# Kernel optimization log

Hardware: AMD Instinct MI355X
Metric: run time of the kernel (lower is better)

The kernel has to match this reference:

```python
import jax, jax.numpy as jnp
import numpy as np

N, L, D, H, HIST = 4, 1024, 1024, 16, 128
HD = D // H          # head_dim = 64
SCALE = D ** 0.5     # note: original scales by sqrt(model_dim), not sqrt(head_dim)


def _band_mask():
    # get_mask: tril XOR tril(diag=-history_len) -> True inside the causal band.
    # masked_fill fills where mask is True, so pass the complement (True outside band).
    r = jnp.arange(L)[:, None]
    c = jnp.arange(L)[None, :]
    band = (c <= r) & (c > r - HIST)  # band of width HIST incl. diagonal
    return jnp.broadcast_to(~band, (N, 1, L, L))


def setup_inputs() -> dict:
    key = jax.random.key(0)
    ks = jax.random.split(key, 8)
    s = 0.02
    return {
        "values": jax.random.normal(ks[0], (N, L, D), jnp.float32),
        "keys": jax.random.normal(ks[1], (N, L, D), jnp.float32),
        "query": jax.random.normal(ks[2], (N, L, D), jnp.float32),
        "mask": _band_mask(),
        "Wv": jax.random.normal(ks[3], (HD, HD), jnp.float32) * s,
        "Wk": jax.random.normal(ks[4], (HD, HD), jnp.float32) * s,
        "Wq": jax.random.normal(ks[5], (HD, HD), jnp.float32) * s,
        "Wo": jax.random.normal(ks[6], (D, D), jnp.float32) * s,
        "bo": jax.random.normal(ks[7], (D,), jnp.float32) * s,
    }


def reference(values, keys, query, mask, Wv, Wk, Wq, Wo, bo):
    n, qlen, _ = query.shape
    # split heads and apply per-head linear projections (nn.Linear: x @ W.T)
    v = values.reshape(n, -1, H, HD) @ Wv.T
    k = keys.reshape(n, -1, H, HD) @ Wk.T
    q = query.reshape(n, qlen, H, HD) @ Wq.T
    # full energy [n, h, q, k]
    energy = jnp.einsum('nqhd,nkhd->nhqk', q, k)
    energy = jnp.where(mask, jnp.float32(-1e20), energy)
    scores = jax.nn.softmax(energy / SCALE, axis=-1)
    # NOTE: faithful to original einsum 'nhql,nlhd->nlhd' (reduces over q):
    # attention[n,l,h,d] = (sum_q scores[n,h,q,l]) * v[n,l,h,d]
    attention = jnp.einsum('nhql,nlhd->nlhd', scores, v)
    out = attention.reshape(n, qlen, D) @ Wo.T + bo
    return out
```

## Files before the change

### kernel.cpp

```cpp
#include <hip/hip_runtime.h>
#include <hip/hip_bf16.h>
#include <math.h>


using short8 = __attribute__((ext_vector_type(8))) short;
using f32x4  = __attribute__((ext_vector_type(4))) float;

__device__ __forceinline__ unsigned short f2bf(float x) {
    unsigned u = __float_as_uint(x);
    u += 0x7FFFu + ((u >> 16) & 1u);
    return (unsigned short)(u >> 16);
}

__global__ __launch_bounds__(256) void k_prep0(const float* __restrict__ Wq,
                                               const float* __restrict__ Wk,
                                               const float* __restrict__ Wv,
                                               const float4* __restrict__ Wo4,
                                               float* __restrict__ w,
                                               ushort4* __restrict__ wob4,
                                               unsigned short* __restrict__ Mrb,
                                               unsigned short* __restrict__ Wvb) {
    const int b = blockIdx.x, tid = threadIdx.x;
    if (b < 1024) {
        int idx = b * 256 + tid;
        float4 v = Wo4[idx];
        ushort4 o; o.x = f2bf(v.x); o.y = f2bf(v.y);
        o.z = f2bf(v.z); o.w = f2bf(v.w);
        wob4[idx] = o;
        if (b < 256) w[b * 256 + tid] = 0.f;
    } else {
        int idx = (b - 1024) * 256 + tid;
        int e = idx >> 6, f = idx & 63;
        float s = 0.f;
#pragma unroll 8
        for (int d = 0; d < 64; ++d) s = fmaf(Wq[d * 64 + e], Wk[d * 64 + f], s);
        Mrb[idx] = f2bf(s * (1.0f / 32.0f));
        Wvb[idx] = f2bf(Wv[idx]);
    }
}

__global__ __launch_bounds__(256) void k_kp(const float* __restrict__ keys,
                                            const unsigned short* __restrict__ Mrb,
                                            unsigned short* __restrict__ kk2p) {
    const int tid = threadIdx.x;
    const long R0 = (long)blockIdx.x * 64;
    const int wv = tid >> 6, lane = tid & 63;
    const int m = lane & 15, ksel = (lane >> 4) * 8;

    const float* ka = keys + (R0 + wv * 16 + m) * 64;
    short8 af[2];
#pragma unroll
    for (int ch = 0; ch < 2; ++ch) {
        float4 x0 = *reinterpret_cast<const float4*>(ka + ch * 32 + ksel);
        float4 x1 = *reinterpret_cast<const float4*>(ka + ch * 32 + ksel + 4);
        short8 a;
        a[0] = (short)f2bf(x0.x); a[1] = (short)f2bf(x0.y);
        a[2] = (short)f2bf(x0.z); a[3] = (short)f2bf(x0.w);
        a[4] = (short)f2bf(x1.x); a[5] = (short)f2bf(x1.y);
        a[6] = (short)f2bf(x1.z); a[7] = (short)f2bf(x1.w);
        af[ch] = a;
    }

    f32x4 acc[4];
#pragma unroll
    for (int fc = 0; fc < 4; ++fc) {
        acc[fc] = f32x4{0.f, 0.f, 0.f, 0.f};
#pragma unroll
        for (int ch = 0; ch < 2; ++ch) {
            short8 bf = *reinterpret_cast<const short8*>(
                Mrb + (size_t)(fc * 16 + m) * 64 + ch * 32 + ksel);
            acc[fc] = __builtin_amdgcn_mfma_f32_16x16x32_bf16(af[ch], bf, acc[fc], 0, 0, 0);
        }
    }

    const long rowb = R0 + wv * 16 + (lane >> 4) * 4;
#pragma unroll
    for (int reg = 0; reg < 4; ++reg) {
        long rg = rowb + reg;
        int hh = (int)(rg & 15);
        int ll = (int)((rg >> 4) & 1023);
        int nn = (int)(rg >> 14);
        unsigned short* orow = kk2p + ((size_t)((nn * 16 + hh) * 1024 + ll)) * 64;
#pragma unroll
        for (int fc = 0; fc < 4; ++fc)
            orow[fc * 16 + m] = f2bf(acc[fc][reg]);
    }
}

__global__ __launch_bounds__(256) void k_w2(const float* __restrict__ query,
                                            const unsigned short* __restrict__ kk2p,
                                            float* __restrict__ w) {
    __shared__ float wloc[192];

    const int tid  = threadIdx.x;
    const int b    = blockIdx.x;
    const int nh   = b & 63;
    const int tile = b >> 6;
    const int h    = nh & 15;
    const int n    = nh >> 4;
    const int t0   = tile * 64;

    if (tid < 192) wloc[tid] = 0.f;
    __syncthreads();

    const int wv = tid >> 6, lane = tid & 63;
    const int m = lane & 15, q4 = lane >> 4, ksel = q4 * 8;

    const float* qrow = query + ((size_t)(n * 1024 + t0 + wv * 16 + m)) * 1024 + h * 64;
    short8 af0, af1;
    {
        float4 x0 = *reinterpret_cast<const float4*>(qrow + ksel);
        float4 x1 = *reinterpret_cast<const float4*>(qrow + ksel + 4);
        float4 y0 = *reinterpret_cast<const float4*>(qrow + 32 + ksel);
        float4 y1 = *reinterpret_cast<const float4*>(qrow + 32 + ksel + 4);
        af0[0] = (short)f2bf(x0.x); af0[1] = (short)f2bf(x0.y);
        af0[2] = (short)f2bf(x0.z); af0[3] = (short)f2bf(x0.w);
        af0[4] = (short)f2bf(x1.x); af0[5] = (short)f2bf(x1.y);
        af0[6] = (short)f2bf(x1.z); af0[7] = (short)f2bf(x1.w);
        af1[0] = (short)f2bf(y0.x); af1[1] = (short)f2bf(y0.y);
        af1[2] = (short)f2bf(y0.z); af1[3] = (short)f2bf(y0.w);
        af1[4] = (short)f2bf(y1.x); af1[5] = (short)f2bf(y1.y);
        af1[6] = (short)f2bf(y1.z); af1[7] = (short)f2bf(y1.w);
    }

    const unsigned short* kb = kk2p + (size_t)nh * 1024 * 64;

    f32x4 acc[12];
#pragma unroll
    for (int ni = 0; ni < 12; ++ni) {
        int l = t0 - 127 + ni * 16 + m;
        int lc = min(max(l, 0), 1023);
        const unsigned short* kp = kb + (size_t)lc * 64 + ksel;
        short8 b0 = *reinterpret_cast<const short8*>(kp);
        short8 b1 = *reinterpret_cast<const short8*>(kp + 32);
        f32x4 a = f32x4{0.f, 0.f, 0.f, 0.f};
        a = __builtin_amdgcn_mfma_f32_16x16x32_bf16(af0, b0, a, 0, 0, 0);
        a = __builtin_amdgcn_mfma_f32_16x16x32_bf16(af1, b1, a, 0, 0, 0);
        acc[ni] = a;
    }

    const int rbase = wv * 16 + q4 * 4;
    float rs[4] = {0.f, 0.f, 0.f, 0.f};
#pragma unroll
    for (int ni = 0; ni < 12; ++ni) {
        const int c = ni * 16 + m;
#pragma unroll
        for (int reg = 0; reg < 4; ++reg) {
            const int rlw = rbase + reg;
            bool valid = (c >= rlw) && (c <= rlw + 127) && (c + t0 >= 127);
            float e = valid ? __expf(acc[ni][reg]) : 0.f;
            acc[ni][reg] = e;
            rs[reg] += e;
        }
    }
#pragma unroll
    for (int reg = 0; reg < 4; ++reg) {
#pragma unroll
        for (int mm = 1; mm < 16; mm <<= 1) rs[reg] += __shfl_xor(rs[reg], mm);
        rs[reg] = 1.0f / rs[reg];
    }
#pragma unroll
    for (int ni = 0; ni < 12; ++ni) {
        float cs = acc[ni][0] * rs[0] + acc[ni][1] * rs[1] +
                   acc[ni][2] * rs[2] + acc[ni][3] * rs[3];
        cs += __shfl_xor(cs, 16);
        cs += __shfl_xor(cs, 32);
        if (lane < 16) atomicAdd(&wloc[ni * 16 + m], cs);
    }
    __syncthreads();

    for (int c = tid; c < 192; c += 256) {
        int l = t0 - 127 + c;
        if (l >= 0 && l < 1024)
            atomicAdd(&w[(size_t)nh * 1024 + l], wloc[c]);
    }
}

__global__ __launch_bounds__(256) void k_ap2(const float* __restrict__ values,
                                             const unsigned short* __restrict__ Wvb,
                                             const float* __restrict__ w,
                                             unsigned short* __restrict__ apb) {
    const int tid = threadIdx.x;
    const long R0 = (long)blockIdx.x * 64;
    const int wv = tid >> 6, lane = tid & 63;
    const int m = lane & 15, ksel = (lane >> 4) * 8;

    const float* va = values + (R0 + wv * 16 + m) * 64;
    short8 af[2];
#pragma unroll
    for (int ch = 0; ch < 2; ++ch) {
        float4 x0 = *reinterpret_cast<const float4*>(va + ch * 32 + ksel);
        float4 x1 = *reinterpret_cast<const float4*>(va + ch * 32 + ksel + 4);
        short8 a;
        a[0] = (short)f2bf(x0.x); a[1] = (short)f2bf(x0.y);
        a[2] = (short)f2bf(x0.z); a[3] = (short)f2bf(x0.w);
        a[4] = (short)f2bf(x1.x); a[5] = (short)f2bf(x1.y);
        a[6] = (short)f2bf(x1.z); a[7] = (short)f2bf(x1.w);
        af[ch] = a;
    }

    f32x4 acc[4];
#pragma unroll
    for (int dc = 0; dc < 4; ++dc) {
        acc[dc] = f32x4{0.f, 0.f, 0.f, 0.f};
#pragma unroll
        for (int ch = 0; ch < 2; ++ch) {
            short8 bf = *reinterpret_cast<const short8*>(
                Wvb + (size_t)(dc * 16 + m) * 64 + ch * 32 + ksel);
            acc[dc] = __builtin_amdgcn_mfma_f32_16x16x32_bf16(af[ch], bf, acc[dc], 0, 0, 0);
        }
    }

    const long rowb = R0 + wv * 16 + (lane >> 4) * 4;
    float wf[4];
#pragma unroll
    for (int reg = 0; reg < 4; ++reg) {
        long rg = rowb + reg;
        int hh = (int)(rg & 15);
        int ll = (int)((rg >> 4) & 1023);
        int nn = (int)(rg >> 14);
        wf[reg] = w[((size_t)(nn * 16 + hh) << 10) + ll];
    }
#pragma unroll
    for (int dc = 0; dc < 4; ++dc)
#pragma unroll
        for (int reg = 0; reg < 4; ++reg)
            apb[(size_t)(rowb + reg) * 64 + dc * 16 + m] = f2bf(acc[dc][reg] * wf[reg]);
}

__global__ __launch_bounds__(256) void k_out_mfma(
    const unsigned short* __restrict__ apb,
    const unsigned short* __restrict__ wob,
    const float* __restrict__ bo,
    float* __restrict__ out) {
    __shared__ unsigned short As[128 * 32];
    __shared__ unsigned short Bs[64 * 32];

    const int tid  = threadIdx.x;
    const int wv   = tid >> 6;
    const int lane = tid & 63;
    const int m    = lane & 15;

    const int by = blockIdx.x & 31;
    const int bx = blockIdx.x >> 5;
    const long arow0 = (long)by * 128;
    const int  bcol0 = bx * 64;

    f32x4 acc[2][4];
#pragma unroll
    for (int mi = 0; mi < 2; ++mi)
#pragma unroll
        for (int ni = 0; ni < 4; ++ni) acc[mi][ni] = f32x4{0.f, 0.f, 0.f, 0.f};

    const int r0s = tid >> 2;
    const int kks = (tid & 3) * 8;

    for (int kt = 0; kt < 32; ++kt) {
        const int k0 = kt * 32;
#pragma unroll
        for (int i = 0; i < 2; ++i) {
            const unsigned short* g =
                apb + (arow0 + i * 64 + r0s) * 1024 + k0 + kks;
            __builtin_amdgcn_global_load_lds(
                (const __attribute__((address_space(1))) unsigned int*)g,
                (__attribute__((address_space(3))) unsigned int*)&As[i * 2048 + wv * 512],
                16, 0, 0);
        }
        {
            const unsigned short* g =
                wob + (size_t)(bcol0 + r0s) * 1024 + k0 + kks;
            __builtin_amdgcn_global_load_lds(
                (const __attribute__((address_space(1))) unsigned int*)g,
                (__attribute__((address_space(3))) unsigned int*)&Bs[wv * 512],
                16, 0, 0);
        }
        __syncthreads();

        const int koff = (lane >> 4) * 8;
        const int rA = wv * 32 + m;
        short8 af[2], bf[4];
#pragma unroll
        for (int mi = 0; mi < 2; ++mi)
            af[mi] = *reinterpret_cast<const short8*>(&As[(rA + mi * 16) * 32 + koff]);
#pragma unroll
        for (int ni = 0; ni < 4; ++ni)
            bf[ni] = *reinterpret_cast<const short8*>(&Bs[(ni * 16 + m) * 32 + koff]);
#pragma unroll
        for (int mi = 0; mi < 2; ++mi)
#pragma unroll
            for (int ni = 0; ni < 4; ++ni)
                acc[mi][ni] = __builtin_amdgcn_mfma_f32_16x16x32_bf16(
                    af[mi], bf[ni], acc[mi][ni], 0, 0, 0);
        __syncthreads();
    }

    const int colb = bcol0 + m;
    const int rowb = (int)arow0 + wv * 32 + (lane >> 4) * 4;
#pragma unroll
    for (int ni = 0; ni < 4; ++ni) {
        const int col = colb + ni * 16;
        const float bias = bo[col];
#pragma unroll
        for (int mi = 0; mi < 2; ++mi) {
            const int row = rowb + mi * 16;
#pragma unroll
            for (int r = 0; r < 4; ++r)
                out[(size_t)(row + r) * 1024 + col] = acc[mi][ni][r] + bias;
        }
    }
}

extern "C" void kernel_launch(void* const* d_in, const int* in_sizes, int n_in,
                              void* d_out, int out_size, void* d_ws, size_t ws_size,
                              hipStream_t stream) {
    const float* values = (const float*)d_in[0];
    const float* keys   = (const float*)d_in[1];
    const float* query  = (const float*)d_in[2];
    const float* Wv     = (const float*)d_in[4];
    const float* Wk     = (const float*)d_in[5];
    const float* Wq     = (const float*)d_in[6];
    const float* Wo     = (const float*)d_in[7];
    const float* bo     = (const float*)d_in[8];
    float* out = (float*)d_out;

    float* w             = (float*)d_ws;
    unsigned short* Mrb  = (unsigned short*)(w + 65536);
    unsigned short* Wvb  = Mrb + 4096;
    unsigned short* wob  = Wvb + 4096;
    unsigned short* kk2p = wob + 1024 * 1024;
    unsigned short* apb  = kk2p + 64 * 1024 * 64;

    k_prep0<<<1040, 256, 0, stream>>>(Wq, Wk, Wv, (const float4*)Wo,
                                      w, (ushort4*)wob, Mrb, Wvb);
    k_kp<<<1024, 256, 0, stream>>>(keys, Mrb, kk2p);
    k_w2<<<1024, 256, 0, stream>>>(query, kk2p, w);
    k_ap2<<<1024, 256, 0, stream>>>(values, Wvb, w, apb);
    k_out_mfma<<<512, 256, 0, stream>>>(apb, wob, bo, out);
}
```

Before: 161.1 us.

## Merge weight prep and key projection into one staging kernel with bf16 query

Combines the weight-prep kernel and the key-projection kernel into one launch. Each key block recomputes the small Wq^T·Wk product with MFMA into shared memory instead of reading a precomputed global matrix. The same launch also pre-converts the query to a head-major bf16 buffer, so the energy kernel loads bf16 fragments directly. This removes one launch and a dependency, but adds redundant per-block matrix work, an extra 8 MB query write and read, and a larger workspace.

New measurement: 158.6 us. About the same (-1.6%).

```diff
diff --git a/kernel.cpp b/kernel.cpp
--- a/kernel.cpp
+++ b/kernel.cpp
@@ -12,82 +12,120 @@
     return (unsigned short)(u >> 16);
 }
 
-__global__ __launch_bounds__(256) void k_prep0(const float* __restrict__ Wq,
+__global__ __launch_bounds__(256) void k_stage(const float* __restrict__ keys,
+                                               const float* __restrict__ query,
+                                               const float* __restrict__ Wq,
                                                const float* __restrict__ Wk,
                                                const float* __restrict__ Wv,
                                                const float4* __restrict__ Wo4,
-                                               float* __restrict__ w,
+                                               unsigned short* __restrict__ kk2p,
+                                               unsigned short* __restrict__ qb,
                                                ushort4* __restrict__ wob4,
-                                               unsigned short* __restrict__ Mrb,
-                                               unsigned short* __restrict__ Wvb) {
+                                               unsigned short* __restrict__ Wvb,
+                                               float* __restrict__ w) {
+    __shared__ unsigned short Ml[64 * 64];
+
     const int b = blockIdx.x, tid = threadIdx.x;
+
     if (b < 1024) {
-        int idx = b * 256 + tid;
+        const int wv = tid >> 6, lane = tid & 63;
+        const int m = lane & 15, q4 = lane >> 4, ksel = q4 * 8;
+
+        {
+            short8 aM0, aM1;
+#pragma unroll
+            for (int j = 0; j < 8; ++j) {
+                aM0[j] = (short)f2bf(Wq[(ksel + j) * 64 + wv * 16 + m]);
+                aM1[j] = (short)f2bf(Wq[(32 + ksel + j) * 64 + wv * 16 + m]);
+            }
+#pragma unroll
+            for (int fc = 0; fc < 4; ++fc) {
+                short8 bM0, bM1;
+#pragma unroll
+                for (int j = 0; j < 8; ++j) {
+                    bM0[j] = (short)f2bf(Wk[(ksel + j) * 64 + fc * 16 + m]);
+                    bM1[j] = (short)f2bf(Wk[(32 + ksel + j) * 64 + fc * 16 + m]);
+                }
+                f32x4 a = f32x4{0.f, 0.f, 0.f, 0.f};
+                a = __builtin_amdgcn_mfma_f32_16x16x32_bf16(aM0, bM0, a, 0, 0, 0);
+                a = __builtin_amdgcn_mfma_f32_16x16x32_bf16(aM1, bM1, a, 0, 0, 0);
+#pragma unroll
+                for (int r = 0; r < 4; ++r)
+                    Ml[(wv * 16 + q4 * 4 + r) * 64 + fc * 16 + m] =
+                        f2bf(a[r] * (1.0f / 32.0f));
+            }
+        }
+        __syncthreads();
+
+        const long R0 = (long)b * 64;
+        const float* ka = keys + (R0 + wv * 16 + m) * 64;
+        short8 af[2];
+#pragma unroll
+        for (int ch = 0; ch < 2; ++ch) {
+            float4 x0 = *reinterpret_cast<const float4*>(ka + ch * 32 + ksel);
+            float4 x1 = *reinterpret_cast<const float4*>(ka + ch * 32 + ksel + 4);
+            short8 a;
+            a[0] = (short)f2bf(x0.x); a[1] = (short)f2bf(x0.y);
+            a[2] = (short)f2bf(x0.z); a[3] = (short)f2bf(x0.w);
+            a[4] = (short)f2bf(x1.x); a[5] = (short)f2bf(x1.y);
+            a[6] = (short)f2bf(x1.z); a[7] = (short)f2bf(x1.w);
+            af[ch] = a;
+        }
+
+        f32x4 acc[4];
+#pragma unroll
+        for (int fc = 0; fc < 4; ++fc) {
+            acc[fc] = f32x4{0.f, 0.f, 0.f, 0.f};
+#pragma unroll
+            for (int ch = 0; ch < 2; ++ch) {
+                short8 bf = *reinterpret_cast<const short8*>(
+                    &Ml[(fc * 16 + m) * 64 + ch * 32 + ksel]);
+                acc[fc] = __builtin_amdgcn_mfma_f32_16x16x32_bf16(af[ch], bf, acc[fc], 0, 0, 0);
+            }
+        }
+
+        const long rowb = R0 + wv * 16 + (lane >> 4) * 4;
+#pragma unroll
+        for (int reg = 0; reg < 4; ++reg) {
+            long rg = rowb + reg;
+            int hh = (int)(rg & 15);
+            int ll = (int)((rg >> 4) & 1023);
+            int nn = (int)(rg >> 14);
+            unsigned short* orow = kk2p + ((size_t)((nn * 16 + hh) * 1024 + ll)) * 64;
+#pragma unroll
+            for (int fc = 0; fc < 4; ++fc)
+                orow[fc * 16 + m] = f2bf(acc[fc][reg]);
+        }
+    } else if (b < 2048) {
+        const int bb = b - 1024;
+        const int tile = bb & 15, nh = bb >> 4, h = nh & 15, n = nh >> 4;
+        const int t0 = tile * 64;
+        const float* qbase = query + ((size_t)(n * 1024 + t0)) * 1024 + h * 64;
+        unsigned short* qout = qb + ((size_t)(nh * 1024 + t0)) * 64;
+#pragma unroll
+        for (int i = 0; i < 4; ++i) {
+            int idx = tid + i * 256;
+            int r = idx >> 4, f0 = (idx & 15) * 4;
+            float4 qv = *reinterpret_cast<const float4*>(qbase + (size_t)r * 1024 + f0);
+            ushort4 qo; qo.x = f2bf(qv.x); qo.y = f2bf(qv.y);
+            qo.z = f2bf(qv.z); qo.w = f2bf(qv.w);
+            *reinterpret_cast<ushort4*>(qout + (size_t)r * 64 + f0) = qo;
+        }
+    } else if (b < 3072) {
+        const int bb = b - 2048;
+        int idx = bb * 256 + tid;
         float4 v = Wo4[idx];
         ushort4 o; o.x = f2bf(v.x); o.y = f2bf(v.y);
         o.z = f2bf(v.z); o.w = f2bf(v.w);
         wob4[idx] = o;
-        if (b < 256) w[b * 256 + tid] = 0.f;
+        if (bb < 256) w[bb * 256 + tid] = 0.f;
     } else {
-        int idx = (b - 1024) * 256 + tid;
-        int e = idx >> 6, f = idx & 63;
-        float s = 0.f;
-#pragma unroll 8
-        for (int d = 0; d < 64; ++d) s = fmaf(Wq[d * 64 + e], Wk[d * 64 + f], s);
-        Mrb[idx] = f2bf(s * (1.0f / 32.0f));
+        int idx = (b - 3072) * 256 + tid;
         Wvb[idx] = f2bf(Wv[idx]);
     }
 }
 
-__global__ __launch_bounds__(256) void k_kp(const float* __restrict__ keys,
-                                            const unsigned short* __restrict__ Mrb,
-                                            unsigned short* __restrict__ kk2p) {
-    const int tid = threadIdx.x;
-    const long R0 = (long)blockIdx.x * 64;
-    const int wv = tid >> 6, lane = tid & 63;
-    const int m = lane & 15, ksel = (lane >> 4) * 8;
-
-    const float* ka = keys + (R0 + wv * 16 + m) * 64;
-    short8 af[2];
-#pragma unroll
-    for (int ch = 0; ch < 2; ++ch) {
-        float4 x0 = *reinterpret_cast<const float4*>(ka + ch * 32 + ksel);
-        float4 x1 = *reinterpret_cast<const float4*>(ka + ch * 32 + ksel + 4);
-        short8 a;
-        a[0] = (short)f2bf(x0.x); a[1] = (short)f2bf(x0.y);
-        a[2] = (short)f2bf(x0.z); a[3] = (short)f2bf(x0.w);
-        a[4] = (short)f2bf(x1.x); a[5] = (short)f2bf(x1.y);
-        a[6] = (short)f2bf(x1.z); a[7] = (short)f2bf(x1.w);
-        af[ch] = a;
-    }
-
-    f32x4 acc[4];
-#pragma unroll
-    for (int fc = 0; fc < 4; ++fc) {
-        acc[fc] = f32x4{0.f, 0.f, 0.f, 0.f};
-#pragma unroll
-        for (int ch = 0; ch < 2; ++ch) {
-            short8 bf = *reinterpret_cast<const short8*>(
-                Mrb + (size_t)(fc * 16 + m) * 64 + ch * 32 + ksel);
-            acc[fc] = __builtin_amdgcn_mfma_f32_16x16x32_bf16(af[ch], bf, acc[fc], 0, 0, 0);
-        }
-    }
-
-    const long rowb = R0 + wv * 16 + (lane >> 4) * 4;
-#pragma unroll
-    for (int reg = 0; reg < 4; ++reg) {
-        long rg = rowb + reg;
-        int hh = (int)(rg & 15);
-        int ll = (int)((rg >> 4) & 1023);
-        int nn = (int)(rg >> 14);
-        unsigned short* orow = kk2p + ((size_t)((nn * 16 + hh) * 1024 + ll)) * 64;
-#pragma unroll
-        for (int fc = 0; fc < 4; ++fc)
-            orow[fc * 16 + m] = f2bf(acc[fc][reg]);
-    }
-}
-
-__global__ __launch_bounds__(256) void k_w2(const float* __restrict__ query,
+__global__ __launch_bounds__(256) void k_w2(const unsigned short* __restrict__ qb,
                                             const unsigned short* __restrict__ kk2p,
                                             float* __restrict__ w) {
     __shared__ float wloc[192];
@@ -96,8 +134,6 @@
     const int b    = blockIdx.x;
     const int nh   = b & 63;
     const int tile = b >> 6;
-    const int h    = nh & 15;
-    const int n    = nh >> 4;
     const int t0   = tile * 64;
 
     if (tid < 192) wloc[tid] = 0.f;
@@ -106,22 +142,9 @@
     const int wv = tid >> 6, lane = tid & 63;
     const int m = lane & 15, q4 = lane >> 4, ksel = q4 * 8;
 
-    const float* qrow = query + ((size_t)(n * 1024 + t0 + wv * 16 + m)) * 1024 + h * 64;
-    short8 af0, af1;
-    {
-        float4 x0 = *reinterpret_cast<const float4*>(qrow + ksel);
-        float4 x1 = *reinterpret_cast<const float4*>(qrow + ksel + 4);
-        float4 y0 = *reinterpret_cast<const float4*>(qrow + 32 + ksel);
-        float4 y1 = *reinterpret_cast<const float4*>(qrow + 32 + ksel + 4);
-        af0[0] = (short)f2bf(x0.x); af0[1] = (short)f2bf(x0.y);
-        af0[2] = (short)f2bf(x0.z); af0[3] = (short)f2bf(x0.w);
-        af0[4] = (short)f2bf(x1.x); af0[5] = (short)f2bf(x1.y);
-        af0[6] = (short)f2bf(x1.z); af0[7] = (short)f2bf(x1.w);
-        af1[0] = (short)f2bf(y0.x); af1[1] = (short)f2bf(y0.y);
-        af1[2] = (short)f2bf(y0.z); af1[3] = (short)f2bf(y0.w);
-        af1[4] = (short)f2bf(y1.x); af1[5] = (short)f2bf(y1.y);
-        af1[6] = (short)f2bf(y1.z); af1[7] = (short)f2bf(y1.w);
-    }
+    const unsigned short* qrow = qb + ((size_t)(nh * 1024 + t0 + wv * 16 + m)) * 64;
+    short8 af0 = *reinterpret_cast<const short8*>(qrow + ksel);
+    short8 af1 = *reinterpret_cast<const short8*>(qrow + 32 + ksel);
 
     const unsigned short* kb = kk2p + (size_t)nh * 1024 * 64;
 
@@ -324,16 +347,15 @@
     float* out = (float*)d_out;
 
     float* w             = (float*)d_ws;
-    unsigned short* Mrb  = (unsigned short*)(w + 65536);
-    unsigned short* Wvb  = Mrb + 4096;
+    unsigned short* Wvb  = (unsigned short*)(w + 65536);
     unsigned short* wob  = Wvb + 4096;
     unsigned short* kk2p = wob + 1024 * 1024;
-    unsigned short* apb  = kk2p + 64 * 1024 * 64;
-
-    k_prep0<<<1040, 256, 0, stream>>>(Wq, Wk, Wv, (const float4*)Wo,
-                                      w, (ushort4*)wob, Mrb, Wvb);
-    k_kp<<<1024, 256, 0, stream>>>(keys, Mrb, kk2p);
-    k_w2<<<1024, 256, 0, stream>>>(query, kk2p, w);
+    unsigned short* qb   = kk2p + 64 * 1024 * 64;
+    unsigned short* apb  = qb + 64 * 1024 * 64;
+
+    k_stage<<<3088, 256, 0, stream>>>(keys, query, Wq, Wk, Wv, (const float4*)Wo,
+                                      kk2p, qb, (ushort4*)wob, Wvb, w);
+    k_w2<<<1024, 256, 0, stream>>>(qb, kk2p, w);
     k_ap2<<<1024, 256, 0, stream>>>(values, Wvb, w, apb);
     k_out_mfma<<<512, 256, 0, stream>>>(apb, wob, bo, out);
 }
```
